# Kernel optimization log

Measured on AMD Instinct MI355X. Metric: run time of the kernel, lower is better.

## Reference

```python
import jax, jax.numpy as jnp
import numpy as np

H_HEADS = 8
HIDDEN = 512
D_K = HIDDEN // H_HEADS


def setup_inputs() -> dict:
    key = jax.random.key(0)
    ks = jax.random.split(key, 16)
    B, T = 4, 1024
    P = 2 * T - 1
    s = 0.02
    inp = {
        "x": jax.random.normal(ks[0], (B, T, HIDDEN), dtype=jnp.float32),
        "pos_emb": jax.random.normal(ks[1], (1, P, HIDDEN), dtype=jnp.float32),
        "Wq": jax.random.normal(ks[2], (HIDDEN, HIDDEN), dtype=jnp.float32) * s,
        "bq": jnp.zeros((HIDDEN,), dtype=jnp.float32),
        "Wk": jax.random.normal(ks[3], (HIDDEN, HIDDEN), dtype=jnp.float32) * s,
        "bk": jnp.zeros((HIDDEN,), dtype=jnp.float32),
        "Wv": jax.random.normal(ks[4], (HIDDEN, HIDDEN), dtype=jnp.float32) * s,
        "bv": jnp.zeros((HIDDEN,), dtype=jnp.float32),
        "Wp": jax.random.normal(ks[5], (HIDDEN, HIDDEN), dtype=jnp.float32) * s,
        "bp": jnp.zeros((HIDDEN,), dtype=jnp.float32),
        "Wo": jax.random.normal(ks[6], (HIDDEN, HIDDEN), dtype=jnp.float32) * s,
        "bo": jnp.zeros((HIDDEN,), dtype=jnp.float32),
        "pos_bias_u": jax.random.normal(ks[7], (H_HEADS, D_K), dtype=jnp.float32) * s,
        "pos_bias_v": jax.random.normal(ks[8], (H_HEADS, D_K), dtype=jnp.float32) * s,
    }
    return inp


def rel_shift(x):
    # x: (B, H, T, P). Transformer-XL relative shift.
    B, H, T, P = x.shape
    x = jnp.pad(x, ((0, 0), (0, 0), (0, 0), (1, 0)))  # (B,H,T,P+1)
    x = x.reshape(B, H, P + 1, T)[:, :, 1:, :]          # drop first row
    return x.reshape(B, H, T, P)


def reference(x, pos_emb, Wq, bq, Wk, bk, Wv, bv, Wp, bp, Wo, bo, pos_bias_u, pos_bias_v):
    B, T, _ = x.shape
    Hh, d = H_HEADS, D_K
    scale = 1.0 / jnp.sqrt(jnp.asarray(d, dtype=x.dtype))

    q = (x @ Wq + bq).reshape(B, T, Hh, d)                       # (B,T,H,d)
    k = (x @ Wk + bk).reshape(B, T, Hh, d).transpose(0, 2, 1, 3)  # (B,H,T,d)
    v = (x @ Wv + bv).reshape(B, T, Hh, d).transpose(0, 2, 1, 3)  # (B,H,T,d)
    P = pos_emb.shape[1]
    p = (pos_emb @ Wp + bp).reshape(pos_emb.shape[0], P, Hh, d).transpose(0, 2, 1, 3)  # (1,H,P,d)

    q_u = (q + pos_bias_u).transpose(0, 2, 1, 3)  # (B,H,T,d)
    q_v = (q + pos_bias_v).transpose(0, 2, 1, 3)  # (B,H,T,d)

    # content-position term with rel-shift (broadcast over batch dim of p)
    matrix_bd = jnp.matmul(q_v, p.transpose(0, 1, 3, 2))  # (B,H,T,P)
    matrix_bd = rel_shift(matrix_bd)[:, :, :, :T] * scale  # (B,H,T,T)

    # content-content term + additive bias, scaled softmax
    scores = jnp.matmul(q_u, k.transpose(0, 1, 3, 2)) * scale + matrix_bd
    attn = jax.nn.softmax(scores.astype(jnp.float32), axis=-1).astype(x.dtype)
    out = jnp.matmul(attn, v)                 # (B,H,T,d)
    out = out.transpose(0, 2, 1, 3).reshape(B, T, Hh * d)
    return out @ Wo + bo
```

## Files before the change

kernel.cpp:

```cpp
#include <hip/hip_runtime.h>
#include <math.h>

#define BATCH 4
#define SEQ   1024
#define HID   512
#define NHEAD 8

typedef unsigned short u16;
typedef unsigned int   u32;
typedef short  short8 __attribute__((ext_vector_type(8)));
typedef float  f32x4  __attribute__((ext_vector_type(4)));

__device__ __forceinline__ u16 f2bf(float x) {
  u32 u = __builtin_bit_cast(u32, x);
  u32 r = (u + 0x7FFFu + ((u >> 16) & 1u)) >> 16;
  return (u16)r;
}
__device__ __forceinline__ float bf2f(u16 h) {
  u32 u = ((u32)h) << 16;
  return __builtin_bit_cast(float, u);
}

__global__ __launch_bounds__(256)
void prep(const float* __restrict__ x, const float* __restrict__ pe,
          const float* __restrict__ w0, const float* __restrict__ w1,
          const float* __restrict__ w2, const float* __restrict__ w3,
          const float* __restrict__ w4,
          u16* __restrict__ xb, u16* __restrict__ peb, u16* __restrict__ wt) {
  __shared__ float t[32][33];
  const int bid = blockIdx.x, tid = threadIdx.x;
  if (bid < 3072) {
    int i = bid * 256 + tid;
    const float* s;
    u16* d;
    if (i < 524288) {
      s = x; d = xb;
    } else {
      i -= 524288;
      if (i >= 262016) return;
      s = pe; d = peb;
    }
    float4 v = *(const float4*)&s[(size_t)i * 4];
    ushort4 o;
    o.x = f2bf(v.x); o.y = f2bf(v.y); o.z = f2bf(v.z); o.w = f2bf(v.w);
    *(ushort4*)&d[(size_t)i * 4] = o;
  } else {
    const int b2 = bid - 3072;
    const int z = b2 >> 8;
    const int rem = b2 & 255;
    const int k0 = (rem & 15) * 32, n0 = (rem >> 4) * 32;
    const float* src = (z == 0) ? w0 : (z == 1) ? w1 : (z == 2) ? w2
                                                     : (z == 3) ? w3 : w4;
    u16* dst = wt + (size_t)z * 512 * 512;
    const int tx = tid & 31, ty = tid >> 5;
#pragma unroll
    for (int r = 0; r < 4; ++r)
      t[ty + 8 * r][tx] = src[(size_t)(k0 + ty + 8 * r) * 512 + n0 + tx];
    __syncthreads();
#pragma unroll
    for (int r = 0; r < 4; ++r)
      dst[(size_t)(n0 + ty + 8 * r) * 512 + k0 + tx] = f2bf(t[tx][ty + 8 * r]);
  }
}

template <int MF, int NF>
__device__ __forceinline__ void gemm_core(const u16* __restrict__ A,
                                          const u16* __restrict__ Bt,
                                          int m0, int n0, u16* As, u16* Bs,
                                          f32x4 (&acc)[MF][NF]) {
  const int tid = threadIdx.x;
  const int wid = tid >> 6, lane = tid & 63;
  const int lr = lane & 15, lg = lane >> 4;
  const int wm = wid >> 1, wn = wid & 1;
  const int srow = tid >> 3, sc = tid & 7;
#pragma unroll
  for (int i = 0; i < MF; ++i)
#pragma unroll
    for (int j = 0; j < NF; ++j) acc[i][j] = (f32x4)0.f;

  for (int kt = 0; kt < 8; ++kt) {
    const int k0 = kt * 64;
    short8 la[MF], lb[NF];
#pragma unroll
    for (int r = 0; r < MF; ++r)
      la[r] = *(const short8*)&A[(size_t)(m0 + srow + 32 * r) * 512 + k0 + sc * 8];
#pragma unroll
    for (int r = 0; r < NF; ++r)
      lb[r] = *(const short8*)&Bt[(size_t)(n0 + srow + 32 * r) * 512 + k0 + sc * 8];
    __syncthreads();
#pragma unroll
    for (int r = 0; r < MF; ++r) {
      int row = srow + 32 * r;
      *(short8*)&As[row * 64 + ((sc ^ (row & 7)) * 8)] = la[r];
    }
#pragma unroll
    for (int r = 0; r < NF; ++r) {
      int row = srow + 32 * r;
      *(short8*)&Bs[row * 64 + ((sc ^ (row & 7)) * 8)] = lb[r];
    }
    __syncthreads();
#pragma unroll
    for (int kc = 0; kc < 2; ++kc) {
      const int ch = kc * 4 + lg;
      short8 af[MF], bfr[NF];
#pragma unroll
      for (int mt = 0; mt < MF; ++mt) {
        int row = wm * (MF * 16) + mt * 16 + lr;
        af[mt] = *(const short8*)&As[row * 64 + ((ch ^ (row & 7)) * 8)];
      }
#pragma unroll
      for (int nt = 0; nt < NF; ++nt) {
        int row = wn * (NF * 16) + nt * 16 + lr;
        bfr[nt] = *(const short8*)&Bs[row * 64 + ((ch ^ (row & 7)) * 8)];
      }
#pragma unroll
      for (int mt = 0; mt < MF; ++mt)
#pragma unroll
        for (int nt = 0; nt < NF; ++nt)
          acc[mt][nt] = __builtin_amdgcn_mfma_f32_16x16x32_bf16(
              af[mt], bfr[nt], acc[mt][nt], 0, 0, 0);
    }
  }
}

__global__ __launch_bounds__(256)
void gemm_qkvp(const u16* __restrict__ xbf, const u16* __restrict__ pebf,
               const u16* __restrict__ wt,
               const float* __restrict__ bq, const float* __restrict__ bk,
               const float* __restrict__ bv, const float* __restrict__ bp,
               u16* __restrict__ qq, u16* __restrict__ kk,
               u16* __restrict__ vt, u16* __restrict__ pp) {
  __shared__ __align__(16) u16 As[128 * 64];
  __shared__ __align__(16) u16 Bs[128 * 64];
  const int z = blockIdx.z;
  if (z == 3 && blockIdx.y >= 16) return;
  const u16* A = (z == 3) ? pebf : xbf;
  const u16* Bt = wt + (size_t)z * 512 * 512;
  const float* bias = (z == 0) ? bq : (z == 1) ? bk : (z == 2) ? bv : bp;
  const int m0 = blockIdx.y * 128, n0 = blockIdx.x * 128;

  f32x4 acc[4][4];
  gemm_core<4, 4>(A, Bt, m0, n0, As, Bs, acc);

  const int tid = threadIdx.x, wid = tid >> 6, lane = tid & 63;
  const int lr = lane & 15, lg = lane >> 4, wm = wid >> 1, wn = wid & 1;
#pragma unroll
  for (int mt = 0; mt < 4; ++mt)
#pragma unroll
    for (int nt = 0; nt < 4; ++nt) {
      const int col = n0 + wn * 64 + nt * 16 + lr;
      const int rb = m0 + wm * 64 + mt * 16 + lg * 4;
      const float bcol = bias[col];
      if (z == 0) {
#pragma unroll
        for (int q = 0; q < 4; ++q)
          qq[(size_t)(rb + q) * 512 + col] = f2bf(acc[mt][nt][q] + bcol);
      } else if (z == 1) {
#pragma unroll
        for (int q = 0; q < 4; ++q)
          kk[(size_t)(rb + q) * 512 + col] = f2bf(acc[mt][nt][q] + bcol);
      } else if (z == 2) {
        ushort4 pk;
        pk.x = f2bf(acc[mt][nt][0] + bcol);
        pk.y = f2bf(acc[mt][nt][1] + bcol);
        pk.z = f2bf(acc[mt][nt][2] + bcol);
        pk.w = f2bf(acc[mt][nt][3] + bcol);
        int bb = rb >> 10, tl = rb & 1023;
        *(ushort4*)&vt[(size_t)((bb * 8 + (col >> 6)) * 64 + (col & 63)) * 1024 + tl] = pk;
      } else {
#pragma unroll
        for (int q = 0; q < 4; ++q)
          if (rb + q < 2047)
            pp[(size_t)(rb + q) * 512 + col] = f2bf(acc[mt][nt][q] + bcol);
      }
    }
}

__global__ __launch_bounds__(256)
void gemm_wo(const u16* __restrict__ ao, const u16* __restrict__ wt,
             const float* __restrict__ bo, float* __restrict__ out) {
  __shared__ __align__(16) u16 As[64 * 64];
  __shared__ __align__(16) u16 Bs[64 * 64];
  const int m0 = blockIdx.y * 64, n0 = blockIdx.x * 64;
  f32x4 acc[2][2];
  gemm_core<2, 2>(ao, wt + (size_t)4 * 512 * 512, m0, n0, As, Bs, acc);
  const int tid = threadIdx.x, wid = tid >> 6, lane = tid & 63;
  const int lr = lane & 15, lg = lane >> 4, wm = wid >> 1, wn = wid & 1;
#pragma unroll
  for (int mt = 0; mt < 2; ++mt)
#pragma unroll
    for (int nt = 0; nt < 2; ++nt) {
      const int col = n0 + wn * 32 + nt * 16 + lr;
      const int rb = m0 + wm * 32 + mt * 16 + lg * 4;
      const float bcol = bo[col];
#pragma unroll
      for (int q = 0; q < 4; ++q)
        out[(size_t)(rb + q) * 512 + col] = acc[mt][nt][q] + bcol;
    }
}

__global__ __launch_bounds__(512)
void attn_mfma(const u16* __restrict__ qP, const float* __restrict__ pbu,
               const float* __restrict__ pbv,
               const u16* __restrict__ kP, const u16* __restrict__ vtP,
               const u16* __restrict__ pP, u16* __restrict__ ao) {
  __shared__ __align__(16) u16 SM[56832];
  u16* Ps = SM + 16384;

  const int tid = threadIdx.x;
  const int wid = tid >> 6, lane = tid & 63;
  const int lr = lane & 15, lg = lane >> 4;
  const int grp = wid >> 2, wq = wid & 3;
  const int t0 = blockIdx.x * 128, h = blockIdx.y, b = blockIdx.z;
  const int base0 = 896 - t0;

  u16* Ksg = SM + grp * 4096;
  u16* Vsg = SM + 8192 + grp * 4096;
  float* wbf = (float*)(SM + 32768) + wid * 1504;
  u16* esw = (u16*)wbf;

  short8 aqu[2][2], aqv[2][2];
#pragma unroll
  for (int kc = 0; kc < 2; ++kc) {
    float4 u0 = *(const float4*)&pbu[h * 64 + kc * 32 + lg * 8];
    float4 u1 = *(const float4*)&pbu[h * 64 + kc * 32 + lg * 8 + 4];
    float4 v0 = *(const float4*)&pbv[h * 64 + kc * 32 + lg * 8];
    float4 v1 = *(const float4*)&pbv[h * 64 + kc * 32 + lg * 8 + 4];
    float ub[8] = {u0.x, u0.y, u0.z, u0.w, u1.x, u1.y, u1.z, u1.w};
    float vb[8] = {v0.x, v0.y, v0.z, v0.w, v1.x, v1.y, v1.z, v1.w};
#pragma unroll
    for (int f = 0; f < 2; ++f) {
      size_t g = (size_t)(b * SEQ + t0 + 32 * wq + 16 * f + lr) * 512 + h * 64 +
                 kc * 32 + lg * 8;
      short8 q8 = *(const short8*)&qP[g];
#pragma unroll
      for (int i = 0; i < 8; ++i) {
        float qf = bf2f((u16)q8[i]);
        aqu[f][kc][i] = (short)f2bf(qf + ub[i]);
        aqv[f][kc][i] = (short)f2bf(qf + vb[i]);
      }
    }
  }
  short8 ones;
#pragma unroll
  for (int i = 0; i < 8; ++i) ones[i] = (short)0x3F80;

  float mrun[2] = {-1e30f, -1e30f};
  f32x4 cL[2], cO[2][4];
#pragma unroll
  for (int f = 0; f < 2; ++f) {
    cL[f] = (f32x4)0.f;
#pragma unroll
    for (int nt = 0; nt < 4; ++nt) cO[f][nt] = (f32x4)0.f;
  }

#pragma unroll
  for (int r = 0; r < 2; ++r) {
    int idx = tid + 512 * r;
    int row = idx >> 3, sc = idx & 7;
    short8 lk = *(const short8*)&kP[(size_t)(b * SEQ + row) * 512 + h * 64 + sc * 8];
    short8 lv = *(const short8*)&vtP[(size_t)((b * 8 + h) * 64 + (row & 63)) * 1024 +
                                     (row >> 6) * 64 + sc * 8];
    *(short8*)&SM[(row >> 6) * 4096 + (row & 63) * 64 + ((sc ^ (row & 7)) * 8)] = lk;
    *(short8*)&SM[8192 + (row >> 6) * 4096 + (row & 63) * 64 + ((sc ^ (row & 7)) * 8)] = lv;
  }
#pragma unroll
  for (int r = 0; r < 4; ++r) {
    int idx = tid + 512 * r;
    int prow = idx >> 3, sc = idx & 7;
    short8 lp = *(const short8*)&pP[(size_t)(base0 + prow) * 512 + h * 64 + sc * 8];
    *(short8*)&Ps[prow * 64 + ((sc ^ (prow & 7)) * 8)] = lp;
  }
  __syncthreads();

  for (int s = 0; s < 8; ++s) {
    short8 nk[2], nv[2], np[2];
    if (s < 7) {
      const int jn = 128 * (s + 1);
#pragma unroll
      for (int r = 0; r < 2; ++r) {
        int idx = tid + 512 * r;
        int row = idx >> 3, sc = idx & 7;
        nk[r] = *(const short8*)&kP[(size_t)(b * SEQ + jn + row) * 512 + h * 64 + sc * 8];
        nv[r] = *(const short8*)&vtP[(size_t)((b * 8 + h) * 64 + (row & 63)) * 1024 +
                                     jn + (row >> 6) * 64 + sc * 8];
        np[r] = *(const short8*)&pP[(size_t)(base0 + 256 + 128 * s + row) * 512 +
                                    h * 64 + sc * 8];
      }
    }

    f32x4 cKT[2][4];
#pragma unroll
    for (int f = 0; f < 2; ++f)
#pragma unroll
      for (int nt = 0; nt < 4; ++nt) cKT[f][nt] = (f32x4)0.f;
    __builtin_amdgcn_s_setprio(1);
#pragma unroll
    for (int kc = 0; kc < 2; ++kc) {
      const int ch = kc * 4 + lg;
#pragma unroll
      for (int nt = 0; nt < 4; ++nt) {
        int krow = nt * 16 + lr;
        short8 bk = *(const short8*)&Ksg[krow * 64 + ((ch ^ (krow & 7)) * 8)];
        cKT[0][nt] = __builtin_amdgcn_mfma_f32_16x16x32_bf16(bk, aqu[0][kc], cKT[0][nt], 0, 0, 0);
        cKT[1][nt] = __builtin_amdgcn_mfma_f32_16x16x32_bf16(bk, aqu[1][kc], cKT[1][nt], 0, 0, 0);
      }
    }
    __builtin_amdgcn_s_setprio(0);

    short8 bvr[2][4];
#pragma unroll
    for (int kc = 0; kc < 2; ++kc) {
      const int ch = kc * 4 + lg;
#pragma unroll
      for (int nt = 0; nt < 4; ++nt) {
        int vr = nt * 16 + lr;
        bvr[kc][nt] = *(const short8*)&Vsg[vr * 64 + ((ch ^ (vr & 7)) * 8)];
      }
    }

    short8 bpc[2][4];
#pragma unroll
    for (int f = 0; f < 2; ++f) {
      const int poff = 112 - 32 * wq - 16 * f + 64 * grp + 128 * s;
      f32x4 cPT[5];
#pragma unroll
      for (int i = 0; i < 5; ++i) cPT[i] = (f32x4)0.f;
      __builtin_amdgcn_s_setprio(1);
#pragma unroll
      for (int kc = 0; kc < 2; ++kc) {
        const int ch = kc * 4 + lg;
        const int swz = (ch ^ (lr & 7)) * 8;
        if (f == 0) {
#pragma unroll
          for (int pt = 0; pt < 5; ++pt) {
            int pos = (poff + pt * 16 + lr) & 255;
            short8 bp = *(const short8*)&Ps[pos * 64 + swz];
            if (pt < 4) bpc[kc][pt] = bp;
            cPT[pt] = __builtin_amdgcn_mfma_f32_16x16x32_bf16(bp, aqv[0][kc], cPT[pt], 0, 0, 0);
          }
        } else {
          int pos = (poff + lr) & 255;
          short8 bp0 = *(const short8*)&Ps[pos * 64 + swz];
          cPT[0] = __builtin_amdgcn_mfma_f32_16x16x32_bf16(bp0, aqv[1][kc], cPT[0], 0, 0, 0);
#pragma unroll
          for (int pt = 1; pt < 5; ++pt)
            cPT[pt] = __builtin_amdgcn_mfma_f32_16x16x32_bf16(bpc[kc][pt - 1], aqv[1][kc], cPT[pt], 0, 0, 0);
        }
      }
      __builtin_amdgcn_s_setprio(0);

#pragma unroll
      for (int pt = 0; pt < 5; ++pt)
        *(f32x4*)&wbf[lr * 84 + pt * 16 + lg * 4] = cPT[pt];
      float sv[4][4];
#pragma unroll
      for (int nt = 0; nt < 4; ++nt)
#pragma unroll
        for (int q = 0; q < 4; ++q)
          sv[nt][q] = 0.125f * (cKT[f][nt][q] +
                                wbf[lr * 84 + 16 * nt + lg * 4 + q + 15 - lr]);

      float tm = sv[0][0];
#pragma unroll
      for (int nt = 0; nt < 4; ++nt)
#pragma unroll
        for (int q = 0; q < 4; ++q) tm = fmaxf(tm, sv[nt][q]);
      tm = fmaxf(tm, __shfl_xor(tm, 16));
      tm = fmaxf(tm, __shfl_xor(tm, 32));
      if (__any(tm > mrun[f] + 8.f)) {
        float mnew = fmaxf(mrun[f], tm);
        float corr = __expf(mrun[f] - mnew);
        mrun[f] = mnew;
        float cc[4];
#pragma unroll
        for (int q = 0; q < 4; ++q)
          cc[q] = __shfl(corr, (lane & 48) | (lg * 4 + q));
#pragma unroll
        for (int q = 0; q < 4; ++q) {
          cL[f][q] *= cc[q];
#pragma unroll
          for (int nt = 0; nt < 4; ++nt) cO[f][nt][q] *= cc[q];
        }
      }

#pragma unroll
      for (int nt = 0; nt < 4; ++nt) {
        float e0 = __expf(sv[nt][0] - mrun[f]);
        float e1 = __expf(sv[nt][1] - mrun[f]);
        float e2 = __expf(sv[nt][2] - mrun[f]);
        float e3 = __expf(sv[nt][3] - mrun[f]);
        uint2 pk;
        pk.x = (u32)f2bf(e0) | ((u32)f2bf(e1) << 16);
        pk.y = (u32)f2bf(e2) | ((u32)f2bf(e3) << 16);
        int g = 2 * nt + (lg >> 1);
        *(uint2*)&esw[lr * 64 + ((g ^ (lr & 7)) * 8) + (lg & 1) * 4] = pk;
      }

      __builtin_amdgcn_s_setprio(1);
#pragma unroll
      for (int kc = 0; kc < 2; ++kc) {
        const int ch = kc * 4 + lg;
        short8 pa = *(const short8*)&esw[lr * 64 + ((ch ^ (lr & 7)) * 8)];
        cL[f] = __builtin_amdgcn_mfma_f32_16x16x32_bf16(pa, ones, cL[f], 0, 0, 0);
#pragma unroll
        for (int nt = 0; nt < 4; ++nt)
          cO[f][nt] = __builtin_amdgcn_mfma_f32_16x16x32_bf16(pa, bvr[kc][nt], cO[f][nt], 0, 0, 0);
      }
      __builtin_amdgcn_s_setprio(0);
    }

    __syncthreads();
    if (s < 7) {
#pragma unroll
      for (int r = 0; r < 2; ++r) {
        int idx = tid + 512 * r;
        int row = idx >> 3, sc = idx & 7;
        *(short8*)&SM[(row >> 6) * 4096 + (row & 63) * 64 + ((sc ^ (row & 7)) * 8)] = nk[r];
        *(short8*)&SM[8192 + (row >> 6) * 4096 + (row & 63) * 64 + ((sc ^ (row & 7)) * 8)] = nv[r];
        int pos = (128 * s + row) & 255;
        *(short8*)&Ps[pos * 64 + ((sc ^ (pos & 7)) * 8)] = np[r];
      }
    }
    __syncthreads();
  }

  float m_c[2][4];
#pragma unroll
  for (int f = 0; f < 2; ++f)
#pragma unroll
    for (int q = 0; q < 4; ++q)
      m_c[f][q] = __shfl(mrun[f], (lane & 48) | (lg * 4 + q));

  float* ob = (float*)SM;
  float* mlb = (float*)(SM + 16384);
  if (grp == 1) {
#pragma unroll
    for (int f = 0; f < 2; ++f) {
#pragma unroll
      for (int nt = 0; nt < 4; ++nt)
#pragma unroll
        for (int q = 0; q < 4; ++q)
          ob[(wq * 32 + 16 * f + 4 * lg + q) * 64 + nt * 16 + lr] = cO[f][nt][q];
      if (lr == 0) {
#pragma unroll
        for (int q = 0; q < 4; ++q) {
          int rr = wq * 32 + 16 * f + 4 * lg + q;
          mlb[rr * 2 + 0] = m_c[f][q];
          mlb[rr * 2 + 1] = cL[f][q];
        }
      }
    }
  }
  __syncthreads();
  if (grp == 0) {
#pragma unroll
    for (int f = 0; f < 2; ++f) {
      float ws0[4], ws1[4];
#pragma unroll
      for (int q = 0; q < 4; ++q) {
        int rr = wq * 32 + 16 * f + 4 * lg + q;
        float m1 = mlb[rr * 2 + 0], l1 = mlb[rr * 2 + 1];
        float M = fmaxf(m_c[f][q], m1);
        float w0 = __expf(m_c[f][q] - M), w1 = __expf(m1 - M);
        float inv = 1.f / (w0 * cL[f][q] + w1 * l1);
        ws0[q] = w0 * inv;
        ws1[q] = w1 * inv;
      }
#pragma unroll
      for (int nt = 0; nt < 4; ++nt)
#pragma unroll
        for (int q = 0; q < 4; ++q) {
          int rr = wq * 32 + 16 * f + 4 * lg + q;
          float o1 = ob[rr * 64 + nt * 16 + lr];
          float val = ws0[q] * cO[f][nt][q] + ws1[q] * o1;
          ao[(size_t)(b * SEQ + t0 + rr) * 512 + h * 64 + nt * 16 + lr] = f2bf(val);
        }
    }
  }
}

extern "C" void kernel_launch(void* const* d_in, const int* in_sizes, int n_in,
                              void* d_out, int out_size, void* d_ws, size_t ws_size,
                              hipStream_t stream) {
  const float* x   = (const float*)d_in[0];
  const float* pe  = (const float*)d_in[1];
  const float* Wq  = (const float*)d_in[2];
  const float* bq  = (const float*)d_in[3];
  const float* Wk  = (const float*)d_in[4];
  const float* bk  = (const float*)d_in[5];
  const float* Wv  = (const float*)d_in[6];
  const float* bv  = (const float*)d_in[7];
  const float* Wp  = (const float*)d_in[8];
  const float* bp  = (const float*)d_in[9];
  const float* Wo  = (const float*)d_in[10];
  const float* bo  = (const float*)d_in[11];
  const float* pbu = (const float*)d_in[12];
  const float* pbv = (const float*)d_in[13];

  char* ws = (char*)d_ws;
  size_t o = 0;
  auto alloc = [&](size_t bytes) { size_t r = o; o += (bytes + 255) & ~(size_t)255; return r; };
  u16* x_bf  = (u16*)(ws + alloc((size_t)4096 * 512 * 2));
  u16* pe_bf = (u16*)(ws + alloc((size_t)2048 * 512 * 2));
  u16* wt    = (u16*)(ws + alloc((size_t)5 * 512 * 512 * 2));
  u16* qq    = (u16*)(ws + alloc((size_t)4096 * 512 * 2));
  u16* kk    = (u16*)(ws + alloc((size_t)4096 * 512 * 2));
  u16* vt    = (u16*)(ws + alloc((size_t)4096 * 512 * 2));
  u16* pp    = (u16*)(ws + alloc((size_t)2048 * 512 * 2));
  u16* ao    = (u16*)(ws + alloc((size_t)4096 * 512 * 2));

  dim3 blk(256);
  prep<<<dim3(4352), blk, 0, stream>>>(x, pe, Wq, Wk, Wv, Wp, Wo, x_bf, pe_bf, wt);
  gemm_qkvp<<<dim3(4, 32, 4), blk, 0, stream>>>(x_bf, pe_bf, wt, bq, bk, bv, bp,
                                                qq, kk, vt, pp);
  attn_mfma<<<dim3(8, NHEAD, BATCH), dim3(512), 0, stream>>>(qq, pbu, pbv, kk, vt,
                                                             pp, ao);
  gemm_wo<<<dim3(8, 64), blk, 0, stream>>>(ao, wt, bo, (float*)d_out);
}
```

Baseline: 77.98 us.

## Interleave both query fragments in attention loop and store position scores as bf16

The attention inner loop is restructured so that both 16-row query fragments are processed together. Their position-score MFMAs, softmax max reductions, exponentials and PV MFMAs are each issued as one interleaved batch instead of running as two sequential passes, which exposes more independent MFMA work per wave. The per-wave scratch buffer used for the relative-shift read-back now holds bf16 instead of fp32 and has a separate slot per fragment, so shared memory use shrinks. The risks are higher register pressure from the doubled live accumulators and a small precision loss on the positional term from rounding it to bf16.

```diff
diff --git a/kernel.cpp b/kernel.cpp
--- a/kernel.cpp
+++ b/kernel.cpp
@@ -204,7 +204,7 @@
                const float* __restrict__ pbv,
                const u16* __restrict__ kP, const u16* __restrict__ vtP,
                const u16* __restrict__ pP, u16* __restrict__ ao) {
-  __shared__ __align__(16) u16 SM[56832];
+  __shared__ __align__(16) u16 SM[55296];
   u16* Ps = SM + 16384;
 
   const int tid = threadIdx.x;
@@ -216,8 +216,7 @@
 
   u16* Ksg = SM + grp * 4096;
   u16* Vsg = SM + 8192 + grp * 4096;
-  float* wbf = (float*)(SM + 32768) + wid * 1504;
-  u16* esw = (u16*)wbf;
+  u16* wbh = SM + 32768 + wid * 2816;
 
   short8 aqu[2][2], aqv[2][2];
 #pragma unroll
@@ -319,57 +318,73 @@
       }
     }
 
-    short8 bpc[2][4];
+    const int poff0 = 112 - 32 * wq + 64 * grp + 128 * s;
+    f32x4 cPT[2][5];
+#pragma unroll
+    for (int f = 0; f < 2; ++f)
+#pragma unroll
+      for (int i = 0; i < 5; ++i) cPT[f][i] = (f32x4)0.f;
+    __builtin_amdgcn_s_setprio(1);
+#pragma unroll
+    for (int kc = 0; kc < 2; ++kc) {
+      const int ch = kc * 4 + lg;
+      const int swz = (ch ^ (lr & 7)) * 8;
+      short8 bpc[4];
+#pragma unroll
+      for (int pt = 0; pt < 5; ++pt) {
+        int pos = (poff0 + pt * 16 + lr) & 255;
+        short8 bp = *(const short8*)&Ps[pos * 64 + swz];
+        if (pt < 4) bpc[pt] = bp;
+        cPT[0][pt] = __builtin_amdgcn_mfma_f32_16x16x32_bf16(bp, aqv[0][kc], cPT[0][pt], 0, 0, 0);
+      }
+      int pos1 = (poff0 - 16 + lr) & 255;
+      short8 bp1 = *(const short8*)&Ps[pos1 * 64 + swz];
+      cPT[1][0] = __builtin_amdgcn_mfma_f32_16x16x32_bf16(bp1, aqv[1][kc], cPT[1][0], 0, 0, 0);
+#pragma unroll
+      for (int pt = 1; pt < 5; ++pt)
+        cPT[1][pt] = __builtin_amdgcn_mfma_f32_16x16x32_bf16(bpc[pt - 1], aqv[1][kc], cPT[1][pt], 0, 0, 0);
+    }
+    __builtin_amdgcn_s_setprio(0);
+
+#pragma unroll
+    for (int f = 0; f < 2; ++f)
+#pragma unroll
+      for (int pt = 0; pt < 5; ++pt) {
+        uint2 pk;
+        pk.x = (u32)f2bf(cPT[f][pt][0]) | ((u32)f2bf(cPT[f][pt][1]) << 16);
+        pk.y = (u32)f2bf(cPT[f][pt][2]) | ((u32)f2bf(cPT[f][pt][3]) << 16);
+        *(uint2*)&wbh[f * 1408 + lr * 88 + pt * 16 + lg * 4] = pk;
+      }
+
+    float sv[2][4][4];
+#pragma unroll
+    for (int f = 0; f < 2; ++f)
+#pragma unroll
+      for (int nt = 0; nt < 4; ++nt)
+#pragma unroll
+        for (int q = 0; q < 4; ++q)
+          sv[f][nt][q] = 0.125f * (cKT[f][nt][q] +
+              bf2f(wbh[f * 1408 + lr * 88 + 16 * nt + lg * 4 + q + 15 - lr]));
+
+    float tmx[2];
 #pragma unroll
     for (int f = 0; f < 2; ++f) {
-      const int poff = 112 - 32 * wq - 16 * f + 64 * grp + 128 * s;
-      f32x4 cPT[5];
-#pragma unroll
-      for (int i = 0; i < 5; ++i) cPT[i] = (f32x4)0.f;
-      __builtin_amdgcn_s_setprio(1);
-#pragma unroll
-      for (int kc = 0; kc < 2; ++kc) {
-        const int ch = kc * 4 + lg;
-        const int swz = (ch ^ (lr & 7)) * 8;
-        if (f == 0) {
-#pragma unroll
-          for (int pt = 0; pt < 5; ++pt) {
-            int pos = (poff + pt * 16 + lr) & 255;
-            short8 bp = *(const short8*)&Ps[pos * 64 + swz];
-            if (pt < 4) bpc[kc][pt] = bp;
-            cPT[pt] = __builtin_amdgcn_mfma_f32_16x16x32_bf16(bp, aqv[0][kc], cPT[pt], 0, 0, 0);
-          }
-        } else {
-          int pos = (poff + lr) & 255;
-          short8 bp0 = *(const short8*)&Ps[pos * 64 + swz];
-          cPT[0] = __builtin_amdgcn_mfma_f32_16x16x32_bf16(bp0, aqv[1][kc], cPT[0], 0, 0, 0);
-#pragma unroll
-          for (int pt = 1; pt < 5; ++pt)
-            cPT[pt] = __builtin_amdgcn_mfma_f32_16x16x32_bf16(bpc[kc][pt - 1], aqv[1][kc], cPT[pt], 0, 0, 0);
-        }
-      }
-      __builtin_amdgcn_s_setprio(0);
-
-#pragma unroll
-      for (int pt = 0; pt < 5; ++pt)
-        *(f32x4*)&wbf[lr * 84 + pt * 16 + lg * 4] = cPT[pt];
-      float sv[4][4];
+      float tm = sv[f][0][0];
 #pragma unroll
       for (int nt = 0; nt < 4; ++nt)
 #pragma unroll
-        for (int q = 0; q < 4; ++q)
-          sv[nt][q] = 0.125f * (cKT[f][nt][q] +
-                                wbf[lr * 84 + 16 * nt + lg * 4 + q + 15 - lr]);
-
-      float tm = sv[0][0];
-#pragma unroll
-      for (int nt = 0; nt < 4; ++nt)
-#pragma unroll
-        for (int q = 0; q < 4; ++q) tm = fmaxf(tm, sv[nt][q]);
-      tm = fmaxf(tm, __shfl_xor(tm, 16));
-      tm = fmaxf(tm, __shfl_xor(tm, 32));
-      if (__any(tm > mrun[f] + 8.f)) {
-        float mnew = fmaxf(mrun[f], tm);
+        for (int q = 0; q < 4; ++q) tm = fmaxf(tm, sv[f][nt][q]);
+      tmx[f] = tm;
+    }
+#pragma unroll
+    for (int f = 0; f < 2; ++f) {
+      tmx[f] = fmaxf(tmx[f], __shfl_xor(tmx[f], 16));
+      tmx[f] = fmaxf(tmx[f], __shfl_xor(tmx[f], 32));
+    }
+#pragma unroll
+    for (int f = 0; f < 2; ++f) {
+      if (__any(tmx[f] > mrun[f] + 8.f)) {
+        float mnew = fmaxf(mrun[f], tmx[f]);
         float corr = __expf(mrun[f] - mnew);
         mrun[f] = mnew;
         float cc[4];
@@ -383,32 +398,38 @@
           for (int nt = 0; nt < 4; ++nt) cO[f][nt][q] *= cc[q];
         }
       }
-
+    }
+
+#pragma unroll
+    for (int f = 0; f < 2; ++f)
 #pragma unroll
       for (int nt = 0; nt < 4; ++nt) {
-        float e0 = __expf(sv[nt][0] - mrun[f]);
-        float e1 = __expf(sv[nt][1] - mrun[f]);
-        float e2 = __expf(sv[nt][2] - mrun[f]);
-        float e3 = __expf(sv[nt][3] - mrun[f]);
+        float e0 = __expf(sv[f][nt][0] - mrun[f]);
+        float e1 = __expf(sv[f][nt][1] - mrun[f]);
+        float e2 = __expf(sv[f][nt][2] - mrun[f]);
+        float e3 = __expf(sv[f][nt][3] - mrun[f]);
         uint2 pk;
         pk.x = (u32)f2bf(e0) | ((u32)f2bf(e1) << 16);
         pk.y = (u32)f2bf(e2) | ((u32)f2bf(e3) << 16);
         int g = 2 * nt + (lg >> 1);
-        *(uint2*)&esw[lr * 64 + ((g ^ (lr & 7)) * 8) + (lg & 1) * 4] = pk;
-      }
-
-      __builtin_amdgcn_s_setprio(1);
-#pragma unroll
-      for (int kc = 0; kc < 2; ++kc) {
-        const int ch = kc * 4 + lg;
-        short8 pa = *(const short8*)&esw[lr * 64 + ((ch ^ (lr & 7)) * 8)];
-        cL[f] = __builtin_amdgcn_mfma_f32_16x16x32_bf16(pa, ones, cL[f], 0, 0, 0);
-#pragma unroll
-        for (int nt = 0; nt < 4; ++nt)
-          cO[f][nt] = __builtin_amdgcn_mfma_f32_16x16x32_bf16(pa, bvr[kc][nt], cO[f][nt], 0, 0, 0);
-      }
-      __builtin_amdgcn_s_setprio(0);
-    }
+        *(uint2*)&wbh[f * 1408 + lr * 64 + ((g ^ (lr & 7)) * 8) + (lg & 1) * 4] = pk;
+      }
+
+    __builtin_amdgcn_s_setprio(1);
+#pragma unroll
+    for (int kc = 0; kc < 2; ++kc) {
+      const int ch = kc * 4 + lg;
+      short8 pa0 = *(const short8*)&wbh[0 * 1408 + lr * 64 + ((ch ^ (lr & 7)) * 8)];
+      short8 pa1 = *(const short8*)&wbh[1 * 1408 + lr * 64 + ((ch ^ (lr & 7)) * 8)];
+      cL[0] = __builtin_amdgcn_mfma_f32_16x16x32_bf16(pa0, ones, cL[0], 0, 0, 0);
+      cL[1] = __builtin_amdgcn_mfma_f32_16x16x32_bf16(pa1, ones, cL[1], 0, 0, 0);
+#pragma unroll
+      for (int nt = 0; nt < 4; ++nt) {
+        cO[0][nt] = __builtin_amdgcn_mfma_f32_16x16x32_bf16(pa0, bvr[kc][nt], cO[0][nt], 0, 0, 0);
+        cO[1][nt] = __builtin_amdgcn_mfma_f32_16x16x32_bf16(pa1, bvr[kc][nt], cO[1][nt], 0, 0, 0);
+      }
+    }
+    __builtin_amdgcn_s_setprio(0);
 
     __syncthreads();
     if (s < 7) {
```

After: 89.96 us. 15.4% more time.
